# Optimization experiments

Hardware: AMD Instinct MI355X
Metric: run time of the kernel (lower is better)

## Reference

```python
import jax, jax.numpy as jnp
import numpy as np

N_VERTS = 778
N_JOINTS_CHAIN = 16  # wrist + 15 articulated joints
N_JOINTS_ALL = 21
PARENTS = np.array([0, 0, 1, 2, 0, 4, 5, 0, 7, 8, 0, 10, 11, 0, 13, 14])


def rodrigues(r):
    """Axis-angle [N,3] -> rotation matrices [N,3,3] (matches torch quat2mat path)."""
    angle = jnp.linalg.norm(r + 1e-8, axis=1, keepdims=True)  # [N,1]
    axis = r / angle
    c = jnp.cos(angle)[..., None]  # [N,1,1]
    s = jnp.sin(angle)[..., None]
    x, y, z = axis[:, 0], axis[:, 1], axis[:, 2]
    zero = jnp.zeros_like(x)
    K = jnp.stack([zero, -z, y,
                   z, zero, -x,
                   -y, x, zero], axis=1).reshape(-1, 3, 3)
    eye = jnp.eye(3, dtype=r.dtype)
    return eye + s * K + (1.0 - c) * jnp.matmul(K, K)


def make_A(R, t):
    """R [B,3,3], t [B,3] -> homogeneous [B,4,4]."""
    B = R.shape[0]
    top = jnp.concatenate([R, t[:, :, None]], axis=2)  # [B,3,4]
    bottom = jnp.broadcast_to(jnp.array([[[0., 0., 0., 1.]]], dtype=R.dtype), (B, 1, 4))
    return jnp.concatenate([top, bottom], axis=1)


def setup_inputs() -> dict:
    key = jax.random.key(0)
    ks = jax.random.split(key, 10)
    B = 8192
    w = jax.random.uniform(ks[9], (N_VERTS, 16), dtype=jnp.float32)
    w = w / jnp.sum(w, axis=1, keepdims=True)  # LBS weights rows sum to 1
    Jr = jax.random.uniform(ks[6], (N_VERTS, N_JOINTS_ALL), dtype=jnp.float32)
    Jr = Jr / jnp.sum(Jr, axis=0, keepdims=True)
    return {
        "beta": jax.random.normal(ks[0], (B, 10), dtype=jnp.float32) * 0.5,
        "theta": jax.random.normal(ks[1], (B, 10), dtype=jnp.float32) * 0.5,
        "wrist_euler": jax.random.normal(ks[2], (B, 3), dtype=jnp.float32) * 0.3,
        "v_template": jax.random.normal(ks[3], (N_VERTS, 3), dtype=jnp.float32) * 0.05,
        "shapedirs": jax.random.normal(ks[4], (10, N_VERTS * 3), dtype=jnp.float32) * 0.01,
        "posedirs": jax.random.normal(ks[5], (135, N_VERTS * 3), dtype=jnp.float32) * 0.01,
        "J_regressor": Jr,
        "hands_comp": jax.random.normal(ks[7], (10, 45), dtype=jnp.float32) * 0.5,
        "hands_mean": jax.random.normal(ks[8], (45,), dtype=jnp.float32) * 0.1,
        "weights": w,
    }


def reference(beta, theta, wrist_euler, v_template, shapedirs, posedirs,
              J_regressor, hands_comp, hands_mean, weights):
    B = beta.shape[0]
    # shape blendshapes
    v_shaped = jnp.matmul(beta, shapedirs).reshape(B, N_VERTS, 3) + v_template
    # joints from shaped template: [B,21,3]
    J = jnp.einsum('bvc,vj->bjc', v_shaped, J_regressor)
    # pca pose -> per-joint axis-angle -> rotation matrices
    euler_pose = jnp.matmul(theta, hands_comp) + hands_mean          # [B,45]
    Rs = rodrigues(euler_pose.reshape(-1, 3)).reshape(B, 15, 3, 3)
    global_rot = rodrigues(wrist_euler.reshape(-1, 3)).reshape(B, 1, 3, 3)
    # pose blendshapes: (Rs - I) flattened
    pose_feature = (Rs - jnp.eye(3, dtype=Rs.dtype)).reshape(B, 135)
    v_posed = v_shaped + jnp.matmul(pose_feature, posedirs).reshape(B, N_VERTS, 3)
    # kinematic chain (16 joints, fixed small loop)
    Rs_all = jnp.concatenate([global_rot, Rs], axis=1)  # [B,16,3,3]
    Jc = J[:, :N_JOINTS_CHAIN, :]
    results = [make_A(Rs_all[:, 0], Jc[:, 0])]
    for i in range(1, N_JOINTS_CHAIN):
        p = int(PARENTS[i])
        A_local = make_A(Rs_all[:, i], Jc[:, i] - Jc[:, p])
        results.append(jnp.matmul(results[p], A_local))
    G = jnp.stack(results, axis=1)  # [B,16,4,4]
    # subtract rest-pose joint locations: A = G - G @ [J;0] in last column
    Jh = jnp.concatenate([Jc, jnp.zeros((B, N_JOINTS_CHAIN, 1), Jc.dtype)], axis=2)
    GJ = jnp.einsum('bjpq,bjq->bjp', G, Jh)  # [B,16,4]
    A = G - jnp.concatenate([jnp.zeros((B, N_JOINTS_CHAIN, 4, 3), G.dtype), GJ[..., None]], axis=3)
    # linear blend skinning
    T = jnp.einsum('vj,bjpq->bvpq', weights, A)  # [B,778,4,4]
    v_posed_h = jnp.concatenate([v_posed, jnp.ones((B, N_VERTS, 1), v_posed.dtype)], axis=2)
    verts = jnp.einsum('bvpq,bvq->bvp', T, v_posed_h)[:, :, :3]
    joints = jnp.einsum('bvc,vj->bjc', verts, J_regressor)  # [B,21,3]
    return joints
```

## Files before the change

### kernel.cpp

```cpp
#include <hip/hip_runtime.h>
#include <math.h>

#define NV 778
#define KROW 2334
#define KTOT 146
#define NCOL 1008
#define NPART 16
#define DTLD 160

__global__ __launch_bounds__(64) void kA_pre(const float* __restrict__ shapedirs,
                                             const float* __restrict__ v_template,
                                             const float* __restrict__ Jreg,
                                             const float* __restrict__ wgt,
                                             float* __restrict__ SJ, float* __restrict__ J0,
                                             float* __restrict__ Q,  float* __restrict__ W2)
{
    const int bid = blockIdx.x;
    const int t = threadIdx.x;
    if (bid < 48) {
        const int j = bid / 3, c = bid % 3;
        float acc[11];
#pragma unroll
        for (int k = 0; k < 11; ++k) acc[k] = 0.f;
        for (int v = t; v < NV; v += 64) {
            const float jr = Jreg[v*21 + j];
            acc[10] += v_template[v*3 + c] * jr;
#pragma unroll
            for (int k = 0; k < 10; ++k)
                acc[k] += shapedirs[(size_t)k*KROW + v*3 + c] * jr;
        }
#pragma unroll
        for (int k = 0; k < 11; ++k) {
            float s = acc[k];
#pragma unroll
            for (int off = 32; off >= 1; off >>= 1) s += __shfl_down(s, off, 64);
            acc[k] = s;
        }
        if (t == 0) {
#pragma unroll
            for (int k = 0; k < 10; ++k) SJ[k*48 + j*3 + c] = acc[k];
            J0[j*3 + c] = acc[10];
        }
    } else if (bid < 384) {
        const int m = bid - 48, j = m >> 4, jj = m & 15;
        float s = 0.f;
        for (int v = t; v < NV; v += 64)
            s += Jreg[v*21 + j] * wgt[v*16 + jj];
#pragma unroll
        for (int off = 32; off >= 1; off >>= 1) s += __shfl_down(s, off, 64);
        if (t == 0) Q[m] = s;
    } else {
        const int gi = (bid - 384)*64 + t;
        if (gi < NV*336) {
            const int v = gi / 336, m = gi % 336;
            const int j = m >> 4, jj = m & 15;
            W2[gi] = Jreg[v*21 + j] * wgt[v*16 + jj];
        }
    }
}

__global__ __launch_bounds__(64) void k_tr(const float* __restrict__ shapedirs,
                                           const float* __restrict__ posedirs,
                                           const float* __restrict__ v_template,
                                           float* __restrict__ DT)
{
    const int v = blockIdx.x;
    const int t = threadIdx.x;
#pragma unroll
    for (int kk = 0; kk < 3; ++kk) {
        const int k = t + kk*64;
        if (k < KTOT) {
            const float* drow = (k < 10)  ? shapedirs + (size_t)k*KROW
                              : (k < 145) ? posedirs + (size_t)(k-10)*KROW
                                          : v_template;
            DT[((size_t)0*NV + v)*DTLD + k] = drow[3*v + 0];
            DT[((size_t)1*NV + v)*DTLD + k] = drow[3*v + 1];
            DT[((size_t)2*NV + v)*DTLD + k] = drow[3*v + 2];
        }
    }
}

__global__ __launch_bounds__(192) void k_pre2(const float* __restrict__ DT,
                                              const float* __restrict__ W2,
                                              float* __restrict__ PKpart)
{
    const int bid = blockIdx.x;
    const int j = bid % 21;
    const int c = (bid / 21) % 3;
    const int s = bid / 63;
    const int k = threadIdx.x;
    if (k >= KTOT) return;
    float acc[16];
#pragma unroll
    for (int q = 0; q < 16; ++q) acc[q] = 0.f;
    const int v0 = s*49, v1 = min(NV, v0 + 49);
    const float* dt = DT + ((size_t)c*NV)*DTLD + k;
    for (int v = v0; v < v1; ++v) {
        const float d = dt[(size_t)v*DTLD];
        const float4* wq = (const float4*)(W2 + (size_t)v*336 + j*16);
        const float4 w0 = wq[0], w1 = wq[1], w2 = wq[2], w3 = wq[3];
        acc[0]  += d*w0.x; acc[1]  += d*w0.y; acc[2]  += d*w0.z; acc[3]  += d*w0.w;
        acc[4]  += d*w1.x; acc[5]  += d*w1.y; acc[6]  += d*w1.z; acc[7]  += d*w1.w;
        acc[8]  += d*w2.x; acc[9]  += d*w2.y; acc[10] += d*w2.z; acc[11] += d*w2.w;
        acc[12] += d*w3.x; acc[13] += d*w3.y; acc[14] += d*w3.z; acc[15] += d*w3.w;
    }
    float* o = PKpart + ((size_t)s*KTOT + k)*NCOL + j*48 + c;
#pragma unroll
    for (int q = 0; q < 16; ++q) o[q*3] = acc[q];
}

__global__ void k_p3(const float* __restrict__ PKpart, float* __restrict__ PK)
{
    const int idx = blockIdx.x*256 + threadIdx.x;
    if (idx < KTOT*NCOL) {
        float s = 0.f;
#pragma unroll
        for (int p = 0; p < NPART; ++p)
            s += PKpart[(size_t)p*KTOT*NCOL + idx];
        PK[idx] = s;
    }
}

__global__ __launch_bounds__(256) void k2_pose(const float* __restrict__ beta,
                                               const float* __restrict__ theta,
                                               const float* __restrict__ wrist,
                                               const float* __restrict__ hc,
                                               const float* __restrict__ hm,
                                               const float* __restrict__ SJ,
                                               const float* __restrict__ J0,
                                               float* __restrict__ coefT,
                                               float* __restrict__ A_g, int B)
{
    __shared__ float Rs[16*144];
    __shared__ float cls[16*148];
    const int t = threadIdx.x;
    const int bl = t >> 4, i = t & 15;
    const int b = blockIdx.x*16 + bl;

    float r0, r1, r2;
    if (i == 0) {
        r0 = wrist[b*3+0]; r1 = wrist[b*3+1]; r2 = wrist[b*3+2];
#pragma unroll
        for (int k = 0; k < 10; ++k) cls[bl*148 + k] = beta[b*10 + k];
        cls[bl*148 + 145] = 1.0f;
    } else {
        const int col = (i-1)*3;
        float e0 = hm[col], e1 = hm[col+1], e2 = hm[col+2];
#pragma unroll
        for (int k = 0; k < 10; ++k) {
            const float th = theta[b*10 + k];
            e0 += th * hc[k*45 + col];
            e1 += th * hc[k*45 + col+1];
            e2 += th * hc[k*45 + col+2];
        }
        r0 = e0; r1 = e1; r2 = e2;
    }
    const float x_ = r0 + 1e-8f, y_ = r1 + 1e-8f, z_ = r2 + 1e-8f;
    const float angle = sqrtf(x_*x_ + y_*y_ + z_*z_);
    const float inv = 1.0f / angle;
    const float x = r0*inv, y = r1*inv, z = r2*inv;
    const float sn = sinf(angle), cs = cosf(angle);
    const float t1 = 1.0f - cs;
    float R[9];
    R[0] = 1.f - t1*(y*y + z*z);
    R[1] = -sn*z + t1*x*y;
    R[2] =  sn*y + t1*x*z;
    R[3] =  sn*z + t1*x*y;
    R[4] = 1.f - t1*(x*x + z*z);
    R[5] = -sn*x + t1*y*z;
    R[6] = -sn*y + t1*x*z;
    R[7] =  sn*x + t1*y*z;
    R[8] = 1.f - t1*(x*x + y*y);
#pragma unroll
    for (int q = 0; q < 9; ++q) Rs[bl*144 + i*9 + q] = R[q];
    if (i > 0) {
#pragma unroll
        for (int q = 0; q < 9; ++q)
            cls[bl*148 + 10 + (i-1)*9 + q] = R[q] - ((q==0||q==4||q==8) ? 1.f : 0.f);
    }
    __syncthreads();

    if (t < KTOT) {
        float tmp[16];
#pragma unroll
        for (int m = 0; m < 16; ++m) tmp[m] = cls[m*148 + t];
        float4* dst = (float4*)(coefT + (size_t)t*B + blockIdx.x*16);
        dst[0] = make_float4(tmp[0],  tmp[1],  tmp[2],  tmp[3]);
        dst[1] = make_float4(tmp[4],  tmp[5],  tmp[6],  tmp[7]);
        dst[2] = make_float4(tmp[8],  tmp[9],  tmp[10], tmp[11]);
        dst[3] = make_float4(tmp[12], tmp[13], tmp[14], tmp[15]);
    }

    if (t < 16) {
        const int b2 = blockIdx.x*16 + t;
        float bt[10];
#pragma unroll
        for (int k = 0; k < 10; ++k) bt[k] = beta[b2*10 + k];
        const float* Rb = Rs + t*144;
        float4* Ab = (float4*)(A_g + (size_t)b2*192);

        auto jointJ = [&](int j, float* o) {
            float j0 = J0[j*3+0], j1 = J0[j*3+1], j2 = J0[j*3+2];
#pragma unroll
            for (int k = 0; k < 10; ++k) {
                j0 += bt[k] * SJ[k*48 + j*3 + 0];
                j1 += bt[k] * SJ[k*48 + j*3 + 1];
                j2 += bt[k] * SJ[k*48 + j*3 + 2];
            }
            o[0] = j0; o[1] = j1; o[2] = j2;
        };

        float G0R[9], J0v[3];
#pragma unroll
        for (int q = 0; q < 9; ++q) G0R[q] = Rb[q];
        jointJ(0, J0v);
#pragma unroll
        for (int r = 0; r < 3; ++r) {
            const float at = J0v[r] - (G0R[r*3+0]*J0v[0] + G0R[r*3+1]*J0v[1] + G0R[r*3+2]*J0v[2]);
            Ab[r] = make_float4(G0R[r*3+0], G0R[r*3+1], G0R[r*3+2], at);
        }
        for (int ch = 0; ch < 5; ++ch) {
            float GpR[9], Gpt[3], Jp[3];
#pragma unroll
            for (int q = 0; q < 9; ++q) GpR[q] = G0R[q];
            Gpt[0]=J0v[0]; Gpt[1]=J0v[1]; Gpt[2]=J0v[2];
            Jp[0]=J0v[0];  Jp[1]=J0v[1];  Jp[2]=J0v[2];
            for (int s = 0; s < 3; ++s) {
                const int j = ch*3 + 1 + s;
                float Rl[9];
                const float* Rj = Rb + j*9;
#pragma unroll
                for (int q = 0; q < 9; ++q) Rl[q] = Rj[q];
                float Jc[3];
                jointJ(j, Jc);
                const float tl0 = Jc[0]-Jp[0], tl1 = Jc[1]-Jp[1], tl2 = Jc[2]-Jp[2];
                float GR[9], Gt[3];
#pragma unroll
                for (int r = 0; r < 3; ++r) {
#pragma unroll
                    for (int cc = 0; cc < 3; ++cc)
                        GR[r*3+cc] = GpR[r*3+0]*Rl[0*3+cc] + GpR[r*3+1]*Rl[1*3+cc] + GpR[r*3+2]*Rl[2*3+cc];
                    Gt[r] = GpR[r*3+0]*tl0 + GpR[r*3+1]*tl1 + GpR[r*3+2]*tl2 + Gpt[r];
                }
#pragma unroll
                for (int r = 0; r < 3; ++r) {
                    const float at = Gt[r] - (GR[r*3+0]*Jc[0] + GR[r*3+1]*Jc[1] + GR[r*3+2]*Jc[2]);
                    Ab[j*3 + r] = make_float4(GR[r*3+0], GR[r*3+1], GR[r*3+2], at);
                }
#pragma unroll
                for (int q = 0; q < 9; ++q) GpR[q] = GR[q];
                Gpt[0]=Gt[0]; Gpt[1]=Gt[1]; Gpt[2]=Gt[2];
                Jp[0]=Jc[0];  Jp[1]=Jc[1];  Jp[2]=Jc[2];
            }
        }
    }
}

__global__ __launch_bounds__(256) void k3_gemm(const float* __restrict__ coefT,
                                               const float* __restrict__ PK,
                                               const float* __restrict__ A_g,
                                               const float* __restrict__ Q,
                                               float* __restrict__ out, int B)
{
    __shared__ float Pex[128*49];
    const int t  = threadIdx.x;
    const int b0 = blockIdx.x * 128;
    const int j  = blockIdx.y;
    const int ci = __builtin_amdgcn_readfirstlane(t >> 6);
    const int bi = t & 63;

    float acc[3][4][2];
#pragma unroll
    for (int u = 0; u < 3; ++u)
#pragma unroll
        for (int cc = 0; cc < 4; ++cc) { acc[u][cc][0] = 0.f; acc[u][cc][1] = 0.f; }

    const float* pkbase = PK + j*48 + 4*ci;
    const float* cbase  = coefT + b0 + 2*bi;

#pragma unroll 2
    for (int k = 0; k < KTOT; ++k) {
        const float2 c2 = *(const float2*)(cbase + (size_t)k*B);
        const float* pr = pkbase + (size_t)k*NCOL;
        const float4 p0 = *(const float4*)(pr);
        const float4 p1 = *(const float4*)(pr + 16);
        const float4 p2 = *(const float4*)(pr + 32);
        acc[0][0][0] += p0.x*c2.x; acc[0][0][1] += p0.x*c2.y;
        acc[0][1][0] += p0.y*c2.x; acc[0][1][1] += p0.y*c2.y;
        acc[0][2][0] += p0.z*c2.x; acc[0][2][1] += p0.z*c2.y;
        acc[0][3][0] += p0.w*c2.x; acc[0][3][1] += p0.w*c2.y;
        acc[1][0][0] += p1.x*c2.x; acc[1][0][1] += p1.x*c2.y;
        acc[1][1][0] += p1.y*c2.x; acc[1][1][1] += p1.y*c2.y;
        acc[1][2][0] += p1.z*c2.x; acc[1][2][1] += p1.z*c2.y;
        acc[1][3][0] += p1.w*c2.x; acc[1][3][1] += p1.w*c2.y;
        acc[2][0][0] += p2.x*c2.x; acc[2][0][1] += p2.x*c2.y;
        acc[2][1][0] += p2.y*c2.x; acc[2][1][1] += p2.y*c2.y;
        acc[2][2][0] += p2.z*c2.x; acc[2][2][1] += p2.z*c2.y;
        acc[2][3][0] += p2.w*c2.x; acc[2][3][1] += p2.w*c2.y;
    }

#pragma unroll
    for (int u = 0; u < 3; ++u)
#pragma unroll
        for (int cc = 0; cc < 4; ++cc)
#pragma unroll
            for (int e = 0; e < 2; ++e)
                Pex[(2*bi + e)*49 + 16*u + 4*ci + cc] = acc[u][cc][e];
    __syncthreads();

    if (t < 128) {
        const int b = b0 + t;
        const float4* Ab = ((const float4*)A_g) + (size_t)b*48;
        const float* Pr = Pex + t*49;
        float jx = 0.f, jy = 0.f, jz = 0.f;
#pragma unroll
        for (int jj = 0; jj < 16; ++jj) {
            const float qv = Q[j*16 + jj];
            const float4 a0 = Ab[jj*3+0];
            const float4 a1 = Ab[jj*3+1];
            const float4 a2 = Ab[jj*3+2];
            const float px = Pr[jj*3+0], py = Pr[jj*3+1], pz = Pr[jj*3+2];
            jx += a0.x*px + a0.y*py + a0.z*pz + a0.w*qv;
            jy += a1.x*px + a1.y*py + a1.z*pz + a1.w*qv;
            jz += a2.x*px + a2.y*py + a2.z*pz + a2.w*qv;
        }
        float* op = out + (size_t)b*63 + j*3;
        op[0] = jx; op[1] = jy; op[2] = jz;
    }
}

extern "C" void kernel_launch(void* const* d_in, const int* in_sizes, int n_in,
                              void* d_out, int out_size, void* d_ws, size_t ws_size,
                              hipStream_t stream) {
    (void)n_in; (void)out_size; (void)ws_size;
    const float* beta       = (const float*)d_in[0];
    const float* theta      = (const float*)d_in[1];
    const float* wrist      = (const float*)d_in[2];
    const float* v_template = (const float*)d_in[3];
    const float* shapedirs  = (const float*)d_in[4];
    const float* posedirs   = (const float*)d_in[5];
    const float* Jreg       = (const float*)d_in[6];
    const float* hc         = (const float*)d_in[7];
    const float* hm         = (const float*)d_in[8];
    const float* wgt        = (const float*)d_in[9];
    float* out = (float*)d_out;
    const int B = in_sizes[0] / 10;

    float* ws = (float*)d_ws;
    size_t off = 0;
    auto alloc = [&](size_t n) { float* p = ws + off; off = (off + n + 63) & ~(size_t)63; return p; };
    float* SJ     = alloc(480);
    float* J0     = alloc(48);
    float* Q      = alloc(336);
    float* W2     = alloc((size_t)NV*336);
    float* DT     = alloc((size_t)3*NV*DTLD);
    float* PKpart = alloc((size_t)NPART*KTOT*NCOL);
    float* PK     = alloc((size_t)KTOT*NCOL);
    float* coefT  = alloc((size_t)KTOT*B);
    float* A_g    = alloc((size_t)B*192);

    const int w2_blocks = (NV*336 + 63)/64;
    kA_pre<<<384 + w2_blocks, 64, 0, stream>>>(shapedirs, v_template, Jreg, wgt, SJ, J0, Q, W2);
    k_tr<<<NV, 64, 0, stream>>>(shapedirs, posedirs, v_template, DT);
    k2_pose<<<(B + 15)/16, 256, 0, stream>>>(beta, theta, wrist, hc, hm, SJ, J0, coefT, A_g, B);
    k_pre2<<<21*3*NPART, 192, 0, stream>>>(DT, W2, PKpart);
    k_p3<<<(KTOT*NCOL + 255)/256, 256, 0, stream>>>(PKpart, PK);
    k3_gemm<<<dim3(B/128, 21), 256, 0, stream>>>(coefT, PK, A_g, Q, out, B);
}
```

Measured before the change: 177.4 us.

## Widen GEMM batch tile, merge transpose into prep kernel, vectorize partial reduction

k3_gemm now gives each thread four batch columns instead of two, so one block covers 256 batches and all 256 threads run the epilogue. The shared-memory staging is laid out column-major for float4 stores. The k_tr transpose is folded into kA_pre as extra blocks, which removes one kernel launch. k_p3 reduces the partial sums with float4 loads. The cost is more accumulator registers per thread and half as many GEMM blocks, which may lower occupancy.

```diff
diff --git a/kernel.cpp b/kernel.cpp
--- a/kernel.cpp
+++ b/kernel.cpp
@@ -9,11 +9,13 @@
 #define DTLD 160
 
 __global__ __launch_bounds__(64) void kA_pre(const float* __restrict__ shapedirs,
+                                             const float* __restrict__ posedirs,
                                              const float* __restrict__ v_template,
                                              const float* __restrict__ Jreg,
                                              const float* __restrict__ wgt,
                                              float* __restrict__ SJ, float* __restrict__ J0,
-                                             float* __restrict__ Q,  float* __restrict__ W2)
+                                             float* __restrict__ Q,  float* __restrict__ W2,
+                                             float* __restrict__ DT, int w2_blocks)
 {
     const int bid = blockIdx.x;
     const int t = threadIdx.x;
@@ -49,33 +51,26 @@
 #pragma unroll
         for (int off = 32; off >= 1; off >>= 1) s += __shfl_down(s, off, 64);
         if (t == 0) Q[m] = s;
-    } else {
+    } else if (bid < 384 + w2_blocks) {
         const int gi = (bid - 384)*64 + t;
         if (gi < NV*336) {
             const int v = gi / 336, m = gi % 336;
             const int j = m >> 4, jj = m & 15;
             W2[gi] = Jreg[v*21 + j] * wgt[v*16 + jj];
         }
-    }
-}
-
-__global__ __launch_bounds__(64) void k_tr(const float* __restrict__ shapedirs,
-                                           const float* __restrict__ posedirs,
-                                           const float* __restrict__ v_template,
-                                           float* __restrict__ DT)
-{
-    const int v = blockIdx.x;
-    const int t = threadIdx.x;
-#pragma unroll
-    for (int kk = 0; kk < 3; ++kk) {
-        const int k = t + kk*64;
-        if (k < KTOT) {
-            const float* drow = (k < 10)  ? shapedirs + (size_t)k*KROW
-                              : (k < 145) ? posedirs + (size_t)(k-10)*KROW
-                                          : v_template;
-            DT[((size_t)0*NV + v)*DTLD + k] = drow[3*v + 0];
-            DT[((size_t)1*NV + v)*DTLD + k] = drow[3*v + 1];
-            DT[((size_t)2*NV + v)*DTLD + k] = drow[3*v + 2];
+    } else {
+        const int v = bid - 384 - w2_blocks;
+#pragma unroll
+        for (int kk = 0; kk < 3; ++kk) {
+            const int k = t + kk*64;
+            if (k < KTOT) {
+                const float* drow = (k < 10)  ? shapedirs + (size_t)k*KROW
+                                  : (k < 145) ? posedirs + (size_t)(k-10)*KROW
+                                              : v_template;
+                DT[((size_t)0*NV + v)*DTLD + k] = drow[3*v + 0];
+                DT[((size_t)1*NV + v)*DTLD + k] = drow[3*v + 1];
+                DT[((size_t)2*NV + v)*DTLD + k] = drow[3*v + 2];
+            }
         }
     }
 }
@@ -109,14 +104,17 @@
     for (int q = 0; q < 16; ++q) o[q*3] = acc[q];
 }
 
-__global__ void k_p3(const float* __restrict__ PKpart, float* __restrict__ PK)
-{
+__global__ void k_p3(const float4* __restrict__ PKpart, float4* __restrict__ PK)
+{
+    const int n4 = KTOT*NCOL/4;
     const int idx = blockIdx.x*256 + threadIdx.x;
-    if (idx < KTOT*NCOL) {
-        float s = 0.f;
-#pragma unroll
-        for (int p = 0; p < NPART; ++p)
-            s += PKpart[(size_t)p*KTOT*NCOL + idx];
+    if (idx < n4) {
+        float4 s = PKpart[idx];
+#pragma unroll
+        for (int p = 1; p < NPART; ++p) {
+            const float4 v = PKpart[(size_t)p*n4 + idx];
+            s.x += v.x; s.y += v.y; s.z += v.z; s.w += v.w;
+        }
         PK[idx] = s;
     }
 }
@@ -262,56 +260,50 @@
                                                const float* __restrict__ Q,
                                                float* __restrict__ out, int B)
 {
-    __shared__ float Pex[128*49];
+    __shared__ float Pex[48*256];
     const int t  = threadIdx.x;
-    const int b0 = blockIdx.x * 128;
+    const int b0 = blockIdx.x * 256;
     const int j  = blockIdx.y;
     const int ci = __builtin_amdgcn_readfirstlane(t >> 6);
     const int bi = t & 63;
 
-    float acc[3][4][2];
-#pragma unroll
-    for (int u = 0; u < 3; ++u)
-#pragma unroll
-        for (int cc = 0; cc < 4; ++cc) { acc[u][cc][0] = 0.f; acc[u][cc][1] = 0.f; }
+    float acc[12][4];
+#pragma unroll
+    for (int m = 0; m < 12; ++m)
+#pragma unroll
+        for (int e = 0; e < 4; ++e) acc[m][e] = 0.f;
 
     const float* pkbase = PK + j*48 + 4*ci;
-    const float* cbase  = coefT + b0 + 2*bi;
+    const float* cbase  = coefT + b0 + 4*bi;
 
 #pragma unroll 2
     for (int k = 0; k < KTOT; ++k) {
-        const float2 c2 = *(const float2*)(cbase + (size_t)k*B);
+        const float4 c4 = *(const float4*)(cbase + (size_t)k*B);
         const float* pr = pkbase + (size_t)k*NCOL;
         const float4 p0 = *(const float4*)(pr);
         const float4 p1 = *(const float4*)(pr + 16);
         const float4 p2 = *(const float4*)(pr + 32);
-        acc[0][0][0] += p0.x*c2.x; acc[0][0][1] += p0.x*c2.y;
-        acc[0][1][0] += p0.y*c2.x; acc[0][1][1] += p0.y*c2.y;
-        acc[0][2][0] += p0.z*c2.x; acc[0][2][1] += p0.z*c2.y;
-        acc[0][3][0] += p0.w*c2.x; acc[0][3][1] += p0.w*c2.y;
-        acc[1][0][0] += p1.x*c2.x; acc[1][0][1] += p1.x*c2.y;
-        acc[1][1][0] += p1.y*c2.x; acc[1][1][1] += p1.y*c2.y;
-        acc[1][2][0] += p1.z*c2.x; acc[1][2][1] += p1.z*c2.y;
-        acc[1][3][0] += p1.w*c2.x; acc[1][3][1] += p1.w*c2.y;
-        acc[2][0][0] += p2.x*c2.x; acc[2][0][1] += p2.x*c2.y;
-        acc[2][1][0] += p2.y*c2.x; acc[2][1][1] += p2.y*c2.y;
-        acc[2][2][0] += p2.z*c2.x; acc[2][2][1] += p2.z*c2.y;
-        acc[2][3][0] += p2.w*c2.x; acc[2][3][1] += p2.w*c2.y;
-    }
-
-#pragma unroll
-    for (int u = 0; u < 3; ++u)
-#pragma unroll
-        for (int cc = 0; cc < 4; ++cc)
-#pragma unroll
-            for (int e = 0; e < 2; ++e)
-                Pex[(2*bi + e)*49 + 16*u + 4*ci + cc] = acc[u][cc][e];
+        const float pv[12] = {p0.x,p0.y,p0.z,p0.w, p1.x,p1.y,p1.z,p1.w, p2.x,p2.y,p2.z,p2.w};
+        const float cv[4]  = {c4.x,c4.y,c4.z,c4.w};
+#pragma unroll
+        for (int m = 0; m < 12; ++m)
+#pragma unroll
+            for (int e = 0; e < 4; ++e)
+                acc[m][e] += pv[m] * cv[e];
+    }
+
+#pragma unroll
+    for (int m = 0; m < 12; ++m) {
+        const int col = 16*(m >> 2) + 4*ci + (m & 3);
+        *(float4*)(&Pex[col*256 + 4*bi]) =
+            make_float4(acc[m][0], acc[m][1], acc[m][2], acc[m][3]);
+    }
     __syncthreads();
 
-    if (t < 128) {
+    {
         const int b = b0 + t;
         const float4* Ab = ((const float4*)A_g) + (size_t)b*48;
-        const float* Pr = Pex + t*49;
+        const float* Pr = Pex + t;
         float jx = 0.f, jy = 0.f, jz = 0.f;
 #pragma unroll
         for (int jj = 0; jj < 16; ++jj) {
@@ -319,7 +311,9 @@
             const float4 a0 = Ab[jj*3+0];
             const float4 a1 = Ab[jj*3+1];
             const float4 a2 = Ab[jj*3+2];
-            const float px = Pr[jj*3+0], py = Pr[jj*3+1], pz = Pr[jj*3+2];
+            const float px = Pr[(jj*3+0)*256];
+            const float py = Pr[(jj*3+1)*256];
+            const float pz = Pr[(jj*3+2)*256];
             jx += a0.x*px + a0.y*py + a0.z*pz + a0.w*qv;
             jy += a1.x*px + a1.y*py + a1.z*pz + a1.w*qv;
             jz += a2.x*px + a2.y*py + a2.z*pz + a2.w*qv;
@@ -360,10 +354,10 @@
     float* A_g    = alloc((size_t)B*192);
 
     const int w2_blocks = (NV*336 + 63)/64;
-    kA_pre<<<384 + w2_blocks, 64, 0, stream>>>(shapedirs, v_template, Jreg, wgt, SJ, J0, Q, W2);
-    k_tr<<<NV, 64, 0, stream>>>(shapedirs, posedirs, v_template, DT);
+    kA_pre<<<384 + w2_blocks + NV, 64, 0, stream>>>(shapedirs, posedirs, v_template,
+                                                    Jreg, wgt, SJ, J0, Q, W2, DT, w2_blocks);
     k2_pose<<<(B + 15)/16, 256, 0, stream>>>(beta, theta, wrist, hc, hm, SJ, J0, coefT, A_g, B);
     k_pre2<<<21*3*NPART, 192, 0, stream>>>(DT, W2, PKpart);
-    k_p3<<<(KTOT*NCOL + 255)/256, 256, 0, stream>>>(PKpart, PK);
-    k3_gemm<<<dim3(B/128, 21), 256, 0, stream>>>(coefT, PK, A_g, Q, out, B);
-}
+    k_p3<<<(KTOT*NCOL/4 + 255)/256, 256, 0, stream>>>((const float4*)PKpart, (float4*)PK);
+    k3_gemm<<<dim3(B/256, 21), 256, 0, stream>>>(coefT, PK, A_g, Q, out, B);
+}
```

Result: no change. 180.0 us (+1.5%).
